# Optimization experiments

Hardware: AMD Instinct MI355X
Metric: run time of the kernel (lower is better)

The kernel has to match this reference:

```python
import jax, jax.numpy as jnp
import numpy as np


def _conv(x, w, b, pad):
    o = jax.lax.conv_general_dilated(x, w, (1, 1), [(pad, pad), (pad, pad)],
                                     dimension_numbers=('NCHW', 'OIHW', 'NCHW'))
    return o + b[None, :, None, None]


def _prelu(x, a):
    return jnp.where(x >= 0, x, a * x)


def _bn(x, g, b):
    # training-mode BatchNorm2d (biased variance, eps=1e-5)
    m = jnp.mean(x, axis=(0, 2, 3), keepdims=True)
    v = jnp.var(x, axis=(0, 2, 3), keepdims=True)
    return (x - m) * jax.lax.rsqrt(v + 1e-5) * g[None, :, None, None] + b[None, :, None, None]


def _maxpool2(x):
    return jax.lax.reduce_window(x, -jnp.inf, jax.lax.max, (1, 1, 2, 2), (1, 1, 2, 2), 'VALID')


def _up2(x):
    # bilinear upsample x2, align_corners=True
    B, C, H, W = x.shape
    Ho, Wo = 2 * H, 2 * W
    ys = jnp.arange(Ho, dtype=x.dtype) * ((H - 1) / (Ho - 1))
    xs = jnp.arange(Wo, dtype=x.dtype) * ((W - 1) / (Wo - 1))
    y0 = jnp.floor(ys).astype(jnp.int32)
    y1 = jnp.minimum(y0 + 1, H - 1)
    wy = (ys - y0.astype(x.dtype))[:, None]
    x0 = jnp.floor(xs).astype(jnp.int32)
    x1 = jnp.minimum(x0 + 1, W - 1)
    wx = xs - x0.astype(x.dtype)
    rows = x[:, :, y0, :] * (1 - wy) + x[:, :, y1, :] * wy  # [B,C,Ho,W]
    return rows[:, :, :, x0] * (1 - wx) + rows[:, :, :, x1] * wx


def _dyn_conv(x, w):
    # per-sample dynamic conv: x [B,1,H,W], w [B,Cout,k,k], pad = k//2 - 1
    # fused as a single grouped conv (groups = B) instead of B*Cout tiny launches
    B, Cout, k, _ = w.shape
    pad = k // 2 - 1
    xi = x.reshape(1, B, x.shape[2], x.shape[3])
    wi = w.reshape(B * Cout, 1, k, k)
    o = jax.lax.conv_general_dilated(xi, wi, (1, 1), [(pad, pad), (pad, pad)],
                                     dimension_numbers=('NCHW', 'OIHW', 'NCHW'),
                                     feature_group_count=B)
    return o.reshape(B, Cout, o.shape[2], o.shape[3])


def _double(x, w1, b1, w2, b2, a1, a2):
    return _prelu(_conv(_prelu(_conv(x, w1, b1, 1), a1), w2, b2, 1), a2)


def _forward(x, w, c1_w, c1_b, d2_w1, d2_b1, d2_w2, d2_b2, d3_w1, d3_b1, d3_w2, d3_b2,
             d4_w1, d4_b1, d4_w2, d4_b2, u3_w1, u3_b1, u3_w2, u3_b2, u2_w1, u2_b1,
             u2_w2, u2_b2, u1_w1, u1_b1, u1_w2, u1_b2, last_w, last_b,
             bn1_g, bn1_b, bn2_g, bn2_b, bn3_g, bn3_b, bn4_g, bn4_b, prelu_a):
    c1 = _prelu(_dyn_conv(x, w), prelu_a[0])          # [B,32,H-1,W-1]
    c1 = _prelu(_conv(c1, c1_w, c1_b, 2), prelu_a[1])  # 4x4 pad 2 -> [B,32,H,W]
    c1 = _bn(c1, bn1_g, bn1_b)
    h = _maxpool2(c1)
    c2 = _bn(_double(h, d2_w1, d2_b1, d2_w2, d2_b2, prelu_a[2], prelu_a[3]), bn2_g, bn2_b)
    h = _maxpool2(c2)
    c3 = _bn(_double(h, d3_w1, d3_b1, d3_w2, d3_b2, prelu_a[4], prelu_a[5]), bn3_g, bn3_b)
    h = _maxpool2(c3)
    h = _bn(_double(h, d4_w1, d4_b1, d4_w2, d4_b2, prelu_a[6], prelu_a[7]), bn4_g, bn4_b)
    h = jnp.concatenate([_up2(h), c3], axis=1)  # 512+256
    h = _double(h, u3_w1, u3_b1, u3_w2, u3_b2, prelu_a[8], prelu_a[9])
    h = jnp.concatenate([_up2(h), c2], axis=1)  # 256+128
    h = _double(h, u2_w1, u2_b1, u2_w2, u2_b2, prelu_a[10], prelu_a[11])
    h = jnp.concatenate([_up2(h), c1], axis=1)  # 128+32
    h = _double(h, u1_w1, u1_b1, u1_w2, u1_b2, prelu_a[12], prelu_a[13])
    return _conv(h, last_w, last_b, 0)


def setup_inputs() -> dict:
    key = jax.random.key(0)
    ks = iter(jax.random.split(key, 32))
    d = {}
    d['x'] = jax.random.normal(next(ks), (8, 1, 256, 256), jnp.float32)
    d['w'] = jax.random.normal(next(ks), (8, 32, 8, 8), jnp.float32) * 0.1
    wspecs = [('c1_w', (32, 32, 4, 4)), ('d2_w1', (128, 32, 3, 3)), ('d2_w2', (128, 128, 3, 3)),
              ('d3_w1', (256, 128, 3, 3)), ('d3_w2', (256, 256, 3, 3)),
              ('d4_w1', (512, 256, 3, 3)), ('d4_w2', (512, 512, 3, 3)),
              ('u3_w1', (256, 768, 3, 3)), ('u3_w2', (256, 256, 3, 3)),
              ('u2_w1', (128, 384, 3, 3)), ('u2_w2', (128, 128, 3, 3)),
              ('u1_w1', (32, 160, 3, 3)), ('u1_w2', (32, 32, 3, 3)), ('last_w', (1, 32, 1, 1))]
    for name, shp in wspecs:
        d[name] = jax.random.normal(next(ks), shp, jnp.float32) * 0.05
        d[name.replace('_w', '_b')] = jnp.zeros((shp[0],), jnp.float32)
    for name, c in [('bn1', 32), ('bn2', 128), ('bn3', 256), ('bn4', 512)]:
        d[name + '_g'] = jnp.ones((c,), jnp.float32)
        d[name + '_b'] = jnp.zeros((c,), jnp.float32)
    d['prelu_a'] = jnp.full((14,), 0.25, jnp.float32)
    return d


def reference(x, w, c1_w, c1_b, d2_w1, d2_b1, d2_w2, d2_b2, d3_w1, d3_b1, d3_w2, d3_b2,
              d4_w1, d4_b1, d4_w2, d4_b2, u3_w1, u3_b1, u3_w2, u3_b2, u2_w1, u2_b1,
              u2_w2, u2_b2, u1_w1, u1_b1, u1_w2, u1_b2, last_w, last_b,
              bn1_g, bn1_b, bn2_g, bn2_b, bn3_g, bn3_b, bn4_g, bn4_b, prelu_a):
    return _forward(x, w, c1_w, c1_b, d2_w1, d2_b1, d2_w2, d2_b2, d3_w1, d3_b1,
                    d3_w2, d3_b2, d4_w1, d4_b1, d4_w2, d4_b2, u3_w1, u3_b1, u3_w2,
                    u3_b2, u2_w1, u2_b1, u2_w2, u2_b2, u1_w1, u1_b1, u1_w2, u1_b2,
                    last_w, last_b, bn1_g, bn1_b, bn2_g, bn2_b, bn3_g, bn3_b,
                    bn4_g, bn4_b, prelu_a)
```

## Files before the change

### kernel.cpp

```cpp
#include <hip/hip_runtime.h>
#include <hip/hip_bf16.h>
#include <cstddef>


typedef _Float16 h16;
typedef __attribute__((ext_vector_type(8))) _Float16 h16x8;
typedef __attribute__((ext_vector_type(4))) float f32x4;
union F8 { uint4 u; h16x8 h; };
union UH { unsigned u; h16 h[2]; };

__device__ __forceinline__ float h2f(unsigned short s) {
    union { h16 h; unsigned short s; } c; c.s = s; return (float)c.h;
}
__device__ __forceinline__ unsigned short f2h(float f) {
    union { h16 h; unsigned short s; } c; c.h = (h16)f; return c.s;
}
__device__ __forceinline__ unsigned pack2(float a, float b) {
    return (unsigned)f2h(a) | ((unsigned)f2h(b) << 16);
}
__device__ __forceinline__ void up8(const uint4& v, float* f) {
    f[0]=h2f(v.x&0xffff); f[1]=h2f(v.x>>16);
    f[2]=h2f(v.y&0xffff); f[3]=h2f(v.y>>16);
    f[4]=h2f(v.z&0xffff); f[5]=h2f(v.z>>16);
    f[6]=h2f(v.w&0xffff); f[7]=h2f(v.w>>16);
}

struct PackDesc { const float* src; h16* dst; int I, T, OB, nGrp; };
struct PackArgs { PackDesc d[13]; int total; };

__global__ __launch_bounds__(256) void k_packall(PackArgs a)
{
    int gid = blockIdx.x * 256 + threadIdx.x;
    if (gid >= a.total) return;
    int li = 0, rel = gid;
    while (rel >= a.d[li].nGrp) { rel -= a.d[li].nGrp; ++li; }
    const PackDesc& D = a.d[li];
    int I8 = D.I >> 3;
    int o  = rel / (D.T * I8);
    int r2 = rel - o * (D.T * I8);
    int t  = r2 / I8;
    int i8 = r2 - t * I8;
    int ob = o / D.OB, om = o - ob * D.OB;
    int mt = om >> 4, m16 = om & 15;
    int chunk = i8 >> 2, quad = i8 & 3;
    int lane = quad * 16 + m16;
    int nch = D.I >> 5;
    size_t grp = ((((size_t)ob * D.T + t) * nch + chunk) * (D.OB >> 4) + mt) * 64 + lane;
    const float* src = D.src + ((size_t)o * D.I + i8 * 8) * D.T + t;
    h16* d = D.dst + grp * 8;
#pragma unroll
    for (int j = 0; j < 8; ++j) d[j] = (h16)src[(size_t)j * D.T];
}

template<int KH, int KW, int PAD, bool UPS, int MT, bool FIN>
__global__ __launch_bounds__(256, 2) void k_conv_mfma(
    const h16* __restrict__ src1, int C1n, int H1, int W1,
    const h16* __restrict__ src2, int C2n,
    int Hin, int Win, int Ho, int Wo,
    const h16* __restrict__ PW, const float* __restrict__ bias,
    const float* __restrict__ pa, int aidx,
    h16* __restrict__ out, int Cout,
    const float* __restrict__ fw, const float* __restrict__ fb,
    float* __restrict__ fout)
{
    constexpr int WINH = 8 + KH - 1, WINW = 32 + KW - 1;
    constexpr int NPIX = WINH * WINW;
    constexpr int NIT  = NPIX * 4;
    constexpr int MAXIT = (NIT + 255) / 256;
    constexpr int TAPS = KH * KW;
    __shared__ unsigned short lds[2][NPIX * 36];

    const int tid = threadIdx.x;
    const int lane = tid & 63, wv = tid >> 6;
    const int quad = lane >> 4, m16 = lane & 15;
    const int nCb = Cout / (16 * MT);
    const int b  = blockIdx.z / nCb, cb = blockIdx.z % nCb;
    const int x0 = blockIdx.x * 32, y0 = blockIdx.y * 8;
    const int Cin = C1n + C2n;
    const int nch = Cin >> 5;
    const int co_base = cb * (16 * MT);
    const int srcH = UPS ? Hin : H1;
    const int srcW = UPS ? Win : W1;

    int lof[MAXIT];
    int g1[MAXIT];
    int fl[MAXIT];
    unsigned fyfx[MAXIT];
    int g2[MAXIT];

    const float ry = UPS ? (float)(H1 - 1) / (float)(Hin - 1) : 0.f;
    const float rx = UPS ? (float)(W1 - 1) / (float)(Win - 1) : 0.f;
    const int W1C = UPS ? W1 * C1n : 0;

#pragma unroll
    for (int it = 0; it < MAXIT; ++it) {
        int i = tid + it * 256;
        if (i >= NIT) { lof[it] = -1; g1[it] = -1; g2[it] = -1; fl[it] = 0; fyfx[it] = 0; continue; }
        int p = i >> 2, q = i & 3;
        int wy = p / WINW, wx = p - wy * WINW;
        int yy = y0 - PAD + wy, xx = x0 - PAD + wx;
        lof[it] = p * 36 + q * 8;
        bool val = (unsigned)yy < (unsigned)srcH && (unsigned)xx < (unsigned)srcW;
        if (UPS) {
            fl[it] = 0; fyfx[it] = 0; g1[it] = -1; g2[it] = -1;
            if (val) {
                float ys = yy * ry, xs = xx * rx;
                int yl0 = (int)ys, xl0 = (int)xs;
                float fy = ys - (float)yl0, fx = xs - (float)xl0;
                g1[it] = ((b * H1 + yl0) * W1 + xl0) * C1n + q * 8;
                fl[it] = (yl0 < H1 - 1 ? 1 : 0) | (xl0 < W1 - 1 ? 2 : 0);
                fyfx[it] = pack2(fy, fx);
                g2[it] = ((b * Hin + yy) * Win + xx) * C2n + q * 8;
            }
        } else {
            fl[it] = 0; fyfx[it] = 0; g2[it] = -1;
            g1[it] = val ? ((b * H1 + yy) * W1 + xx) * C1n + q * 8 : -1;
        }
    }

    f32x4 acc[MT][4];
#pragma unroll
    for (int i = 0; i < MT; ++i)
#pragma unroll
        for (int j = 0; j < 4; ++j) acc[i][j] = (f32x4){0.f, 0.f, 0.f, 0.f};

    auto stage = [&](int c0, unsigned short* buf) {
        if (UPS && c0 < C1n) {
#pragma unroll
            for (int it = 0; it < MAXIT; ++it) {
                int lo = lof[it];
                if (lo < 0) continue;
                uint2 lo8 = {0u, 0u}, hi8 = {0u, 0u};
                int g = g1[it];
                if (g >= 0) {
                    const h16* p00 = src1 + g + c0;
                    int oy = (fl[it] & 1) ? W1C : 0;
                    int ox = (fl[it] & 2) ? C1n : 0;
                    F8 v00, v01, v10, v11;
                    v00.u = *(const uint4*)(p00);
                    v01.u = *(const uint4*)(p00 + ox);
                    v10.u = *(const uint4*)(p00 + oy);
                    v11.u = *(const uint4*)(p00 + oy + ox);
                    UH t; t.u = fyfx[it];
                    h16 fy = t.h[0], fx = t.h[1];
                    h16x8 r0 = v00.h + (v10.h - v00.h) * fy;
                    h16x8 r1 = v01.h + (v11.h - v01.h) * fy;
                    F8 rr; rr.h = r0 + (r1 - r0) * fx;
                    lo8 = make_uint2(rr.u.x, rr.u.y);
                    hi8 = make_uint2(rr.u.z, rr.u.w);
                }
                *(uint2*)&buf[lo] = lo8;
                *(uint2*)&buf[lo + 4] = hi8;
            }
        } else if (UPS) {
            int cs = c0 - C1n;
#pragma unroll
            for (int it = 0; it < MAXIT; ++it) {
                int lo = lof[it];
                if (lo < 0) continue;
                uint4 v = {0u, 0u, 0u, 0u};
                int g = g2[it];
                if (g >= 0) v = *(const uint4*)(src2 + g + cs);
                *(uint2*)&buf[lo] = make_uint2(v.x, v.y);
                *(uint2*)&buf[lo + 4] = make_uint2(v.z, v.w);
            }
        } else {
#pragma unroll
            for (int it = 0; it < MAXIT; ++it) {
                int lo = lof[it];
                if (lo < 0) continue;
                uint4 v = {0u, 0u, 0u, 0u};
                int g = g1[it];
                if (g >= 0) v = *(const uint4*)(src1 + g + c0);
                *(uint2*)&buf[lo] = make_uint2(v.x, v.y);
                *(uint2*)&buf[lo + 4] = make_uint2(v.z, v.w);
            }
        }
    };

    const uint4* PW4 = (const uint4*)PW;
    auto sweep = [&](int ci, const unsigned short* buf) {
        size_t abase = (((size_t)cb * TAPS) * nch + ci) * (MT * 64) + lane;
        const size_t astep = (size_t)nch * (MT * 64);
#pragma unroll
        for (int kx = 0; kx < KW; ++kx) {
            F8 a[KH][MT];
#pragma unroll
            for (int ky = 0; ky < KH; ++ky)
#pragma unroll
                for (int mt = 0; mt < MT; ++mt)
                    a[ky][mt].u = PW4[abase + (size_t)(ky * KW + kx) * astep + mt * 64];
#pragma unroll
            for (int wr = 0; wr < 2 + KH - 1; ++wr) {
#pragma unroll
                for (int cg = 0; cg < 2; ++cg) {
                    int row = (wv << 1) + wr;
                    int col = (cg << 4) + m16;
                    int li = (row * WINW + col + kx) * 36 + quad * 8;
                    F8 bf;
                    ((uint2*)&bf)[0] = *(const uint2*)&buf[li];
                    ((uint2*)&bf)[1] = *(const uint2*)&buf[li + 4];
#pragma unroll
                    for (int ky = 0; ky < KH; ++ky) {
                        int ntr = wr - ky;
                        if (ntr < 0 || ntr > 1) continue;
                        int nt = (ntr << 1) + cg;
#pragma unroll
                        for (int mt = 0; mt < MT; ++mt)
                            acc[mt][nt] = __builtin_amdgcn_mfma_f32_16x16x32_f16(
                                a[ky][mt].h, bf.h, acc[mt][nt], 0, 0, 0);
                    }
                }
            }
        }
    };

    stage(0, lds[0]);
    __syncthreads();
    for (int ci = 0; ci < nch; ++ci) {
        int p = ci & 1;
        if (ci + 1 < nch) stage((ci + 1) << 5, lds[p ^ 1]);
        sweep(ci, lds[p]);
        __syncthreads();
    }

    const float alpha = pa[aidx];
    float fin_acc[4] = {0.f, 0.f, 0.f, 0.f};
#pragma unroll
    for (int mt = 0; mt < MT; ++mt) {
        int co = co_base + mt * 16 + quad * 4;
        float4 bi = *(const float4*)(bias + co);
        float4 fw4 = {0.f, 0.f, 0.f, 0.f};
        if (FIN) fw4 = *(const float4*)(fw + co);
#pragma unroll
        for (int nt = 0; nt < 4; ++nt) {
            int y = y0 + (wv << 1) + (nt >> 1);
            int x = x0 + ((nt & 1) << 4) + m16;
            float v0 = acc[mt][nt][0] + bi.x;
            float v1 = acc[mt][nt][1] + bi.y;
            float v2 = acc[mt][nt][2] + bi.z;
            float v3 = acc[mt][nt][3] + bi.w;
            v0 = v0 >= 0.f ? v0 : alpha * v0;
            v1 = v1 >= 0.f ? v1 : alpha * v1;
            v2 = v2 >= 0.f ? v2 : alpha * v2;
            v3 = v3 >= 0.f ? v3 : alpha * v3;
            if (FIN) {
                fin_acc[nt] += v0 * fw4.x + v1 * fw4.y + v2 * fw4.z + v3 * fw4.w;
            } else {
                uint2 r; r.x = pack2(v0, v1); r.y = pack2(v2, v3);
                *(uint2*)(out + ((size_t)((b * Ho + y) * Wo + x)) * Cout + co) = r;
            }
        }
    }
    if (FIN) {
        float fb0 = fb[0];
#pragma unroll
        for (int nt = 0; nt < 4; ++nt) {
            float p = fin_acc[nt];
            p += __shfl_xor(p, 16);
            p += __shfl_xor(p, 32);
            if (quad == 0) {
                int y = y0 + (wv << 1) + (nt >> 1);
                int x = x0 + ((nt & 1) << 4) + m16;
                fout[(size_t)(b * Ho + y) * Wo + x] = p + fb0;
            }
        }
    }
}

__global__ __launch_bounds__(256) void k_dynconv(
    const float* __restrict__ x,
    const float* __restrict__ w,
    const float* __restrict__ pa,
    h16* __restrict__ out)
{
    __shared__ float wl[2048];
    int b = blockIdx.y;
    for (int j = threadIdx.x; j < 2048; j += 256) {
        int t = j >> 5, co = j & 31;
        wl[j] = w[((size_t)(b * 32 + co)) * 64 + t];
    }
    __syncthreads();
    int idx = blockIdx.x * 256 + threadIdx.x;
    if (idx >= 65025) return;
    int py = idx / 255, px = idx - py * 255;
    float acc[32];
#pragma unroll
    for (int c = 0; c < 32; ++c) acc[c] = 0.f;
    const float* xp = x + (size_t)b * 65536;
#pragma unroll
    for (int ky = 0; ky < 8; ++ky) {
        int iy = py + ky - 3;
        if ((unsigned)iy >= 256u) continue;
        const float* row = xp + iy * 256;
#pragma unroll
        for (int kx = 0; kx < 8; ++kx) {
            int ix = px + kx - 3;
            if ((unsigned)ix >= 256u) continue;
            float v = row[ix];
            const float4* wr = (const float4*)&wl[(ky * 8 + kx) * 32];
#pragma unroll
            for (int cg = 0; cg < 8; ++cg) {
                float4 wv = wr[cg];
                acc[cg*4+0] += v * wv.x; acc[cg*4+1] += v * wv.y;
                acc[cg*4+2] += v * wv.z; acc[cg*4+3] += v * wv.w;
            }
        }
    }
    float a = pa[0];
    h16* op = out + ((size_t)(b * 65025 + idx)) * 32;
#pragma unroll
    for (int cg = 0; cg < 4; ++cg) {
        float v[8];
#pragma unroll
        for (int k = 0; k < 8; ++k) {
            float t = acc[cg * 8 + k];
            v[k] = t >= 0.f ? t : a * t;
        }
        uint4 r;
        r.x = pack2(v[0], v[1]); r.y = pack2(v[2], v[3]);
        r.z = pack2(v[4], v[5]); r.w = pack2(v[6], v[7]);
        *(uint4*)(op + cg * 8) = r;
    }
}

__global__ __launch_bounds__(256) void k_bnstats(
    const h16* __restrict__ x, int C, int N, float* __restrict__ sums)
{
    __shared__ float ls[1024];
    for (int j = threadIdx.x; j < 2 * C; j += 256) ls[j] = 0.f;
    __syncthreads();
    int start = blockIdx.x * 256 + threadIdx.x;
    int stride = gridDim.x * 256;
    int c = start & (C - 1);
    float s = 0.f, q = 0.f;
    for (int i = start; i < N; i += stride) {
        float v = h2f(((const unsigned short*)x)[i]);
        s += v; q += v * v;
    }
    atomicAdd(&ls[c], s);
    atomicAdd(&ls[C + c], q);
    __syncthreads();
    for (int j = threadIdx.x; j < 2 * C; j += 256) atomicAdd(&sums[j], ls[j]);
}

__global__ void k_bnfin(
    const float* __restrict__ sums, const float* __restrict__ g,
    const float* __restrict__ bta, int C, float invN, float* __restrict__ sc)
{
    int c = threadIdx.x;
    if (c >= C) return;
    float mean = sums[c] * invN;
    float var  = sums[C + c] * invN - mean * mean;
    float s    = g[c] / sqrtf(var + 1e-5f);
    sc[c]      = s;
    sc[C + c]  = bta[c] - mean * s;
}

__global__ __launch_bounds__(256) void k_bnapply_pool(
    h16* __restrict__ x, h16* __restrict__ pooled,
    int Hin, int Win, int C, int lc8, int lwo, int count,
    const float* __restrict__ sc)
{
    int idx = blockIdx.x * 256 + threadIdx.x;
    if (idx >= count) return;
    int b = blockIdx.y;
    int c8 = idx & ((1 << lc8) - 1);
    int t  = idx >> lc8;
    int ox = t & ((1 << lwo) - 1);
    int oy = t >> lwo;
    int cb = c8 * 8;
    float s[8], sh[8];
#pragma unroll
    for (int k = 0; k < 8; ++k) { s[k] = sc[cb + k]; sh[k] = sc[C + cb + k]; }
    h16* p = x + ((size_t)((b * Hin + oy * 2) * Win + ox * 2)) * C + cb;
    size_t rs = (size_t)Win * C;
    uint4 v00 = *(const uint4*)p;
    uint4 v01 = *(const uint4*)(p + C);
    uint4 v10 = *(const uint4*)(p + rs);
    uint4 v11 = *(const uint4*)(p + rs + C);
    float a[8], bb[8], c[8], d[8], m[8];
    up8(v00, a); up8(v01, bb); up8(v10, c); up8(v11, d);
#pragma unroll
    for (int k = 0; k < 8; ++k) {
        a[k]  = a[k]  * s[k] + sh[k];
        bb[k] = bb[k] * s[k] + sh[k];
        c[k]  = c[k]  * s[k] + sh[k];
        d[k]  = d[k]  * s[k] + sh[k];
        m[k]  = fmaxf(fmaxf(a[k], bb[k]), fmaxf(c[k], d[k]));
    }
    uint4 r;
    r.x = pack2(a[0],a[1]);  r.y = pack2(a[2],a[3]);  r.z = pack2(a[4],a[5]);  r.w = pack2(a[6],a[7]);
    *(uint4*)p = r;
    r.x = pack2(bb[0],bb[1]); r.y = pack2(bb[2],bb[3]); r.z = pack2(bb[4],bb[5]); r.w = pack2(bb[6],bb[7]);
    *(uint4*)(p + C) = r;
    r.x = pack2(c[0],c[1]);  r.y = pack2(c[2],c[3]);  r.z = pack2(c[4],c[5]);  r.w = pack2(c[6],c[7]);
    *(uint4*)(p + rs) = r;
    r.x = pack2(d[0],d[1]);  r.y = pack2(d[2],d[3]);  r.z = pack2(d[4],d[5]);  r.w = pack2(d[6],d[7]);
    *(uint4*)(p + rs + C) = r;
    r.x = pack2(m[0],m[1]);  r.y = pack2(m[2],m[3]);  r.z = pack2(m[4],m[5]);  r.w = pack2(m[6],m[7]);
    int Wo = 1 << lwo;
    *(uint4*)(pooled + ((size_t)((b * (Hin >> 1) + oy)) * Wo + ox) * C + cb) = r;
}

__global__ __launch_bounds__(256) void k_bnapply(
    h16* __restrict__ x, int C, int N8, const float* __restrict__ sc)
{
    __shared__ float ls[1024];
    for (int j = threadIdx.x; j < 2 * C; j += 256) ls[j] = sc[j];
    __syncthreads();
    int idx = blockIdx.x * 256 + threadIdx.x;
    if (idx >= N8) return;
    int cb = (idx << 3) & (C - 1);
    h16* p = x + (size_t)idx * 8;
    uint4 v = *(const uint4*)p;
    float f[8];
    up8(v, f);
    uint4 r;
    float o[8];
#pragma unroll
    for (int k = 0; k < 8; ++k) o[k] = f[k] * ls[cb + k] + ls[C + cb + k];
    r.x = pack2(o[0], o[1]); r.y = pack2(o[2], o[3]);
    r.z = pack2(o[4], o[5]); r.w = pack2(o[6], o[7]);
    *(uint4*)p = r;
}

extern "C" void kernel_launch(void* const* d_in, const int* in_sizes, int n_in,
                              void* d_out, int out_size, void* d_ws, size_t ws_size,
                              hipStream_t stream)
{
    const float* x      = (const float*)d_in[0];
    const float* w      = (const float*)d_in[1];
    const float* c1_w   = (const float*)d_in[2];
    const float* c1_b   = (const float*)d_in[3];
    const float* d2_w1  = (const float*)d_in[4];
    const float* d2_b1  = (const float*)d_in[5];
    const float* d2_w2  = (const float*)d_in[6];
    const float* d2_b2  = (const float*)d_in[7];
    const float* d3_w1  = (const float*)d_in[8];
    const float* d3_b1  = (const float*)d_in[9];
    const float* d3_w2  = (const float*)d_in[10];
    const float* d3_b2  = (const float*)d_in[11];
    const float* d4_w1  = (const float*)d_in[12];
    const float* d4_b1  = (const float*)d_in[13];
    const float* d4_w2  = (const float*)d_in[14];
    const float* d4_b2  = (const float*)d_in[15];
    const float* u3_w1  = (const float*)d_in[16];
    const float* u3_b1  = (const float*)d_in[17];
    const float* u3_w2  = (const float*)d_in[18];
    const float* u3_b2  = (const float*)d_in[19];
    const float* u2_w1  = (const float*)d_in[20];
    const float* u2_b1  = (const float*)d_in[21];
    const float* u2_w2  = (const float*)d_in[22];
    const float* u2_b2  = (const float*)d_in[23];
    const float* u1_w1  = (const float*)d_in[24];
    const float* u1_b1  = (const float*)d_in[25];
    const float* u1_w2  = (const float*)d_in[26];
    const float* u1_b2  = (const float*)d_in[27];
    const float* last_w = (const float*)d_in[28];
    const float* last_b = (const float*)d_in[29];
    const float* bn1_g  = (const float*)d_in[30];
    const float* bn1_b  = (const float*)d_in[31];
    const float* bn2_g  = (const float*)d_in[32];
    const float* bn2_b  = (const float*)d_in[33];
    const float* bn3_g  = (const float*)d_in[34];
    const float* bn3_b  = (const float*)d_in[35];
    const float* bn4_g  = (const float*)d_in[36];
    const float* bn4_b  = (const float*)d_in[37];
    const float* pa     = (const float*)d_in[38];
    float* out = (float*)d_out;

    h16* A0 = (h16*)d_ws;
    h16* C1 = A0;
    h16* C2 = A0 + 16777216;
    h16* C3 = A0 + 33554432;
    h16* A  = A0 + 41943040;
    h16* B  = A0 + 58720256;
    h16* PWb= A0 + 75497472;
    float* SUMS = (float*)(A0 + 83126272);
    float* SC   = SUMS + 2048;
    size_t need = (size_t)83126272 * 2 + 3072 * 4;
    if (ws_size < need) return;

    h16* pw_c1   = PWb;
    h16* pw_d2w1 = PWb + 16384;
    h16* pw_d2w2 = PWb + 53248;
    h16* pw_d3w1 = PWb + 200704;
    h16* pw_d3w2 = PWb + 495616;
    h16* pw_d4w1 = PWb + 1085440;
    h16* pw_d4w2 = PWb + 2265088;
    h16* pw_u3w1 = PWb + 4624384;
    h16* pw_u3w2 = PWb + 6393856;
    h16* pw_u2w1 = PWb + 6983680;
    h16* pw_u2w2 = PWb + 7426048;
    h16* pw_u1w1 = PWb + 7573504;
    h16* pw_u1w2 = PWb + 7619584;

    dim3 blk(256);

    hipMemsetAsync(SUMS, 0, 2048 * sizeof(float), stream);

    PackArgs pk;
    auto mk = [](const float* s, h16* d, int I, int T, int O, int OB) {
        return PackDesc{s, d, I, T, OB, (I >> 3) * T * O};
    };
    pk.d[0]  = mk(c1_w,  pw_c1,   32, 16, 32, 32);
    pk.d[1]  = mk(d2_w1, pw_d2w1, 32,  9, 128, 64);
    pk.d[2]  = mk(d2_w2, pw_d2w2, 128, 9, 128, 64);
    pk.d[3]  = mk(d3_w1, pw_d3w1, 128, 9, 256, 64);
    pk.d[4]  = mk(d3_w2, pw_d3w2, 256, 9, 256, 64);
    pk.d[5]  = mk(d4_w1, pw_d4w1, 256, 9, 512, 32);
    pk.d[6]  = mk(d4_w2, pw_d4w2, 512, 9, 512, 32);
    pk.d[7]  = mk(u3_w1, pw_u3w1, 768, 9, 256, 64);
    pk.d[8]  = mk(u3_w2, pw_u3w2, 256, 9, 256, 64);
    pk.d[9]  = mk(u2_w1, pw_u2w1, 384, 9, 128, 64);
    pk.d[10] = mk(u2_w2, pw_u2w2, 128, 9, 128, 64);
    pk.d[11] = mk(u1_w1, pw_u1w1, 160, 9, 32, 32);
    pk.d[12] = mk(u1_w2, pw_u1w2, 32,  9, 32, 32);
    pk.total = 0;
    for (int i = 0; i < 13; ++i) pk.total += pk.d[i].nGrp;
    k_packall<<<dim3((pk.total + 255) / 256), blk, 0, stream>>>(pk);

    const float* NF = nullptr;
    float* NFO = nullptr;

    k_dynconv<<<dim3(255, 8), blk, 0, stream>>>(x, w, pa, A);
    k_conv_mfma<4,4,2,false,2,false><<<dim3(8, 32, 8), blk, 0, stream>>>(
        A, 32, 255, 255, nullptr, 0, 255, 255, 256, 256,
        pw_c1, c1_b, pa, 1, C1, 32, NF, NF, NFO);
    k_bnstats<<<dim3(1024), blk, 0, stream>>>(C1, 32, 16777216, SUMS);
    k_bnfin<<<dim3(1), dim3(512), 0, stream>>>(SUMS, bn1_g, bn1_b, 32, 32.f / 16777216.f, SC);
    k_bnapply_pool<<<dim3(256, 8), blk, 0, stream>>>(C1, B, 256, 256, 32, 2, 7, 65536, SC);

    k_conv_mfma<3,3,1,false,4,false><<<dim3(4, 16, 16), blk, 0, stream>>>(
        B, 32, 128, 128, nullptr, 0, 128, 128, 128, 128,
        pw_d2w1, d2_b1, pa, 2, A, 128, NF, NF, NFO);
    k_conv_mfma<3,3,1,false,4,false><<<dim3(4, 16, 16), blk, 0, stream>>>(
        A, 128, 128, 128, nullptr, 0, 128, 128, 128, 128,
        pw_d2w2, d2_b2, pa, 3, C2, 128, NF, NF, NFO);
    k_bnstats<<<dim3(1024), blk, 0, stream>>>(C2, 128, 16777216, SUMS + 64);
    k_bnfin<<<dim3(1), dim3(512), 0, stream>>>(SUMS + 64, bn2_g, bn2_b, 128, 128.f / 16777216.f, SC);
    k_bnapply_pool<<<dim3(256, 8), blk, 0, stream>>>(C2, B, 128, 128, 128, 4, 6, 65536, SC);

    k_conv_mfma<3,3,1,false,4,false><<<dim3(2, 8, 32), blk, 0, stream>>>(
        B, 128, 64, 64, nullptr, 0, 64, 64, 64, 64,
        pw_d3w1, d3_b1, pa, 4, A, 256, NF, NF, NFO);
    k_conv_mfma<3,3,1,false,4,false><<<dim3(2, 8, 32), blk, 0, stream>>>(
        A, 256, 64, 64, nullptr, 0, 64, 64, 64, 64,
        pw_d3w2, d3_b2, pa, 5, C3, 256, NF, NF, NFO);
    k_bnstats<<<dim3(1024), blk, 0, stream>>>(C3, 256, 8388608, SUMS + 320);
    k_bnfin<<<dim3(1), dim3(512), 0, stream>>>(SUMS + 320, bn3_g, bn3_b, 256, 256.f / 8388608.f, SC);
    k_bnapply_pool<<<dim3(128, 8), blk, 0, stream>>>(C3, B, 64, 64, 256, 5, 5, 32768, SC);

    k_conv_mfma<3,3,1,false,2,false><<<dim3(1, 4, 128), blk, 0, stream>>>(
        B, 256, 32, 32, nullptr, 0, 32, 32, 32, 32,
        pw_d4w1, d4_b1, pa, 6, A, 512, NF, NF, NFO);
    k_conv_mfma<3,3,1,false,2,false><<<dim3(1, 4, 128), blk, 0, stream>>>(
        A, 512, 32, 32, nullptr, 0, 32, 32, 32, 32,
        pw_d4w2, d4_b2, pa, 7, B, 512, NF, NF, NFO);
    k_bnstats<<<dim3(1024), blk, 0, stream>>>(B, 512, 4194304, SUMS + 832);
    k_bnfin<<<dim3(1), dim3(512), 0, stream>>>(SUMS + 832, bn4_g, bn4_b, 512, 512.f / 4194304.f, SC);
    k_bnapply<<<dim3(2048), blk, 0, stream>>>(B, 512, 524288, SC);

    k_conv_mfma<3,3,1,true,4,false><<<dim3(2, 8, 32), blk, 0, stream>>>(
        B, 512, 32, 32, C3, 256, 64, 64, 64, 64,
        pw_u3w1, u3_b1, pa, 8, A, 256, NF, NF, NFO);
    k_conv_mfma<3,3,1,false,4,false><<<dim3(2, 8, 32), blk, 0, stream>>>(
        A, 256, 64, 64, nullptr, 0, 64, 64, 64, 64,
        pw_u3w2, u3_b2, pa, 9, B, 256, NF, NF, NFO);

    k_conv_mfma<3,3,1,true,4,false><<<dim3(4, 16, 16), blk, 0, stream>>>(
        B, 256, 64, 64, C2, 128, 128, 128, 128, 128,
        pw_u2w1, u2_b1, pa, 10, A, 128, NF, NF, NFO);
    k_conv_mfma<3,3,1,false,4,false><<<dim3(4, 16, 16), blk, 0, stream>>>(
        A, 128, 128, 128, nullptr, 0, 128, 128, 128, 128,
        pw_u2w2, u2_b2, pa, 11, B, 128, NF, NF, NFO);

    k_conv_mfma<3,3,1,true,2,false><<<dim3(8, 32, 8), blk, 0, stream>>>(
        B, 128, 128, 128, C1, 32, 256, 256, 256, 256,
        pw_u1w1, u1_b1, pa, 12, A, 32, NF, NF, NFO);
    k_conv_mfma<3,3,1,false,2,true><<<dim3(8, 32, 8), blk, 0, stream>>>(
        A, 32, 256, 256, nullptr, 0, 256, 256, 256, 256,
        pw_u1w2, u1_b2, pa, 13, B, 32, last_w, last_b, out);
}
```

Before: 1.186 ms.

## Fuse BatchNorm statistics into conv epilogue and fold finalize into apply kernels

The conv kernel gains a BNS template flag. When it is set, the epilogue accumulates per-channel sum and sum of squares of the post-PReLU outputs, reduces them with wave shuffles and LDS atomics, then adds them to global sums with atomics. This removes four separate bnstats passes that reread large fp16 activations, and the bnfin launches are folded into the apply kernels, which now compute scale and shift per thread. In exchange the epilogue carries extra registers and atomics, and every apply thread redundantly recomputes sqrt and divide. Statistics are now summed in fp32 before fp16 rounding, which changes numerics slightly.

```diff
diff --git a/kernel.cpp b/kernel.cpp
--- a/kernel.cpp
+++ b/kernel.cpp
@@ -52,7 +52,7 @@
     for (int j = 0; j < 8; ++j) d[j] = (h16)src[(size_t)j * D.T];
 }
 
-template<int KH, int KW, int PAD, bool UPS, int MT, bool FIN>
+template<int KH, int KW, int PAD, bool UPS, int MT, bool FIN, bool BNS>
 __global__ __launch_bounds__(256, 2) void k_conv_mfma(
     const h16* __restrict__ src1, int C1n, int H1, int W1,
     const h16* __restrict__ src2, int C2n,
@@ -61,7 +61,7 @@
     const float* __restrict__ pa, int aidx,
     h16* __restrict__ out, int Cout,
     const float* __restrict__ fw, const float* __restrict__ fb,
-    float* __restrict__ fout)
+    float* __restrict__ fout, float* __restrict__ gsums)
 {
     constexpr int WINH = 8 + KH - 1, WINW = 32 + KW - 1;
     constexpr int NPIX = WINH * WINW;
@@ -69,6 +69,7 @@
     constexpr int MAXIT = (NIT + 255) / 256;
     constexpr int TAPS = KH * KW;
     __shared__ unsigned short lds[2][NPIX * 36];
+    __shared__ float bnred[128];
 
     const int tid = threadIdx.x;
     const int lane = tid & 63, wv = tid >> 6;
@@ -216,6 +217,7 @@
     };
 
     stage(0, lds[0]);
+    if (BNS && tid < 128) bnred[tid] = 0.f;
     __syncthreads();
     for (int ci = 0; ci < nch; ++ci) {
         int p = ci & 1;
@@ -226,6 +228,13 @@
 
     const float alpha = pa[aidx];
     float fin_acc[4] = {0.f, 0.f, 0.f, 0.f};
+    float lsum[MT][4], lsq[MT][4];
+    if (BNS) {
+#pragma unroll
+        for (int mt = 0; mt < MT; ++mt)
+#pragma unroll
+            for (int j = 0; j < 4; ++j) { lsum[mt][j] = 0.f; lsq[mt][j] = 0.f; }
+    }
 #pragma unroll
     for (int mt = 0; mt < MT; ++mt) {
         int co = co_base + mt * 16 + quad * 4;
@@ -244,6 +253,12 @@
             v1 = v1 >= 0.f ? v1 : alpha * v1;
             v2 = v2 >= 0.f ? v2 : alpha * v2;
             v3 = v3 >= 0.f ? v3 : alpha * v3;
+            if (BNS) {
+                lsum[mt][0] += v0; lsq[mt][0] += v0 * v0;
+                lsum[mt][1] += v1; lsq[mt][1] += v1 * v1;
+                lsum[mt][2] += v2; lsq[mt][2] += v2 * v2;
+                lsum[mt][3] += v3; lsq[mt][3] += v3 * v3;
+            }
             if (FIN) {
                 fin_acc[nt] += v0 * fw4.x + v1 * fw4.y + v2 * fw4.z + v3 * fw4.w;
             } else {
@@ -264,6 +279,30 @@
                 int x = x0 + ((nt & 1) << 4) + m16;
                 fout[(size_t)(b * Ho + y) * Wo + x] = p + fb0;
             }
+        }
+    }
+    if (BNS) {
+#pragma unroll
+        for (int mt = 0; mt < MT; ++mt)
+#pragma unroll
+            for (int j = 0; j < 4; ++j) {
+                float s = lsum[mt][j], q = lsq[mt][j];
+                s += __shfl_xor(s, 1); q += __shfl_xor(q, 1);
+                s += __shfl_xor(s, 2); q += __shfl_xor(q, 2);
+                s += __shfl_xor(s, 4); q += __shfl_xor(q, 4);
+                s += __shfl_xor(s, 8); q += __shfl_xor(q, 8);
+                if (m16 == 0) {
+                    int ch = mt * 16 + quad * 4 + j;
+                    atomicAdd(&bnred[ch], s);
+                    atomicAdd(&bnred[64 + ch], q);
+                }
+            }
+        __syncthreads();
+        if (tid < 16 * MT)
+            atomicAdd(&gsums[co_base + tid], bnred[tid]);
+        else if (tid < 32 * MT) {
+            int ch = tid - 16 * MT;
+            atomicAdd(&gsums[Cout + co_base + ch], bnred[64 + ch]);
         }
     }
 }
@@ -324,43 +363,11 @@
     }
 }
 
-__global__ __launch_bounds__(256) void k_bnstats(
-    const h16* __restrict__ x, int C, int N, float* __restrict__ sums)
-{
-    __shared__ float ls[1024];
-    for (int j = threadIdx.x; j < 2 * C; j += 256) ls[j] = 0.f;
-    __syncthreads();
-    int start = blockIdx.x * 256 + threadIdx.x;
-    int stride = gridDim.x * 256;
-    int c = start & (C - 1);
-    float s = 0.f, q = 0.f;
-    for (int i = start; i < N; i += stride) {
-        float v = h2f(((const unsigned short*)x)[i]);
-        s += v; q += v * v;
-    }
-    atomicAdd(&ls[c], s);
-    atomicAdd(&ls[C + c], q);
-    __syncthreads();
-    for (int j = threadIdx.x; j < 2 * C; j += 256) atomicAdd(&sums[j], ls[j]);
-}
-
-__global__ void k_bnfin(
-    const float* __restrict__ sums, const float* __restrict__ g,
-    const float* __restrict__ bta, int C, float invN, float* __restrict__ sc)
-{
-    int c = threadIdx.x;
-    if (c >= C) return;
-    float mean = sums[c] * invN;
-    float var  = sums[C + c] * invN - mean * mean;
-    float s    = g[c] / sqrtf(var + 1e-5f);
-    sc[c]      = s;
-    sc[C + c]  = bta[c] - mean * s;
-}
-
 __global__ __launch_bounds__(256) void k_bnapply_pool(
     h16* __restrict__ x, h16* __restrict__ pooled,
     int Hin, int Win, int C, int lc8, int lwo, int count,
-    const float* __restrict__ sc)
+    const float* __restrict__ sums, const float* __restrict__ g,
+    const float* __restrict__ beta, float invN)
 {
     int idx = blockIdx.x * 256 + threadIdx.x;
     if (idx >= count) return;
@@ -372,7 +379,14 @@
     int cb = c8 * 8;
     float s[8], sh[8];
 #pragma unroll
-    for (int k = 0; k < 8; ++k) { s[k] = sc[cb + k]; sh[k] = sc[C + cb + k]; }
+    for (int k = 0; k < 8; ++k) {
+        int c = cb + k;
+        float mean = sums[c] * invN;
+        float var  = sums[C + c] * invN - mean * mean;
+        float sc   = g[c] / sqrtf(var + 1e-5f);
+        s[k]  = sc;
+        sh[k] = beta[c] - mean * sc;
+    }
     h16* p = x + ((size_t)((b * Hin + oy * 2) * Win + ox * 2)) * C + cb;
     size_t rs = (size_t)Win * C;
     uint4 v00 = *(const uint4*)p;
@@ -404,14 +418,23 @@
 }
 
 __global__ __launch_bounds__(256) void k_bnapply(
-    h16* __restrict__ x, int C, int N8, const float* __restrict__ sc)
+    h16* __restrict__ x, int C, int N8,
+    const float* __restrict__ sums, const float* __restrict__ g,
+    const float* __restrict__ beta, float invN)
 {
-    __shared__ float ls[1024];
-    for (int j = threadIdx.x; j < 2 * C; j += 256) ls[j] = sc[j];
-    __syncthreads();
     int idx = blockIdx.x * 256 + threadIdx.x;
     if (idx >= N8) return;
     int cb = (idx << 3) & (C - 1);
+    float s[8], sh[8];
+#pragma unroll
+    for (int k = 0; k < 8; ++k) {
+        int c = cb + k;
+        float mean = sums[c] * invN;
+        float var  = sums[C + c] * invN - mean * mean;
+        float sc   = g[c] / sqrtf(var + 1e-5f);
+        s[k]  = sc;
+        sh[k] = beta[c] - mean * sc;
+    }
     h16* p = x + (size_t)idx * 8;
     uint4 v = *(const uint4*)p;
     float f[8];
@@ -419,7 +442,7 @@
     uint4 r;
     float o[8];
 #pragma unroll
-    for (int k = 0; k < 8; ++k) o[k] = f[k] * ls[cb + k] + ls[C + cb + k];
+    for (int k = 0; k < 8; ++k) o[k] = f[k] * s[k] + sh[k];
     r.x = pack2(o[0], o[1]); r.y = pack2(o[2], o[3]);
     r.z = pack2(o[4], o[5]); r.w = pack2(o[6], o[7]);
     *(uint4*)p = r;
@@ -478,8 +501,7 @@
     h16* B  = A0 + 58720256;
     h16* PWb= A0 + 75497472;
     float* SUMS = (float*)(A0 + 83126272);
-    float* SC   = SUMS + 2048;
-    size_t need = (size_t)83126272 * 2 + 3072 * 4;
+    size_t need = (size_t)83126272 * 2 + 2048 * 4;
     if (ws_size < need) return;
 
     h16* pw_c1   = PWb;
@@ -496,8 +518,9 @@
     h16* pw_u1w1 = PWb + 7573504;
     h16* pw_u1w2 = PWb + 7619584;
 
+    float* S1 = SUMS, *S2 = SUMS + 64, *S3 = SUMS + 320, *S4 = SUMS + 832;
+
     dim3 blk(256);
-
     hipMemsetAsync(SUMS, 0, 2048 * sizeof(float), stream);
 
     PackArgs pk;
@@ -525,61 +548,57 @@
     float* NFO = nullptr;
 
     k_dynconv<<<dim3(255, 8), blk, 0, stream>>>(x, w, pa, A);
-    k_conv_mfma<4,4,2,false,2,false><<<dim3(8, 32, 8), blk, 0, stream>>>(
+    k_conv_mfma<4,4,2,false,2,false,true><<<dim3(8, 32, 8), blk, 0, stream>>>(
         A, 32, 255, 255, nullptr, 0, 255, 255, 256, 256,
-        pw_c1, c1_b, pa, 1, C1, 32, NF, NF, NFO);
-    k_bnstats<<<dim3(1024), blk, 0, stream>>>(C1, 32, 16777216, SUMS);
-    k_bnfin<<<dim3(1), dim3(512), 0, stream>>>(SUMS, bn1_g, bn1_b, 32, 32.f / 16777216.f, SC);
-    k_bnapply_pool<<<dim3(256, 8), blk, 0, stream>>>(C1, B, 256, 256, 32, 2, 7, 65536, SC);
-
-    k_conv_mfma<3,3,1,false,4,false><<<dim3(4, 16, 16), blk, 0, stream>>>(
+        pw_c1, c1_b, pa, 1, C1, 32, NF, NF, NFO, S1);
+    k_bnapply_pool<<<dim3(256, 8), blk, 0, stream>>>(
+        C1, B, 256, 256, 32, 2, 7, 65536, S1, bn1_g, bn1_b, 32.f / 16777216.f);
+
+    k_conv_mfma<3,3,1,false,4,false,false><<<dim3(4, 16, 16), blk, 0, stream>>>(
         B, 32, 128, 128, nullptr, 0, 128, 128, 128, 128,
-        pw_d2w1, d2_b1, pa, 2, A, 128, NF, NF, NFO);
-    k_conv_mfma<3,3,1,false,4,false><<<dim3(4, 16, 16), blk, 0, stream>>>(
+        pw_d2w1, d2_b1, pa, 2, A, 128, NF, NF, NFO, NFO);
+    k_conv_mfma<3,3,1,false,4,false,true><<<dim3(4, 16, 16), blk, 0, stream>>>(
         A, 128, 128, 128, nullptr, 0, 128, 128, 128, 128,
-        pw_d2w2, d2_b2, pa, 3, C2, 128, NF, NF, NFO);
-    k_bnstats<<<dim3(1024), blk, 0, stream>>>(C2, 128, 16777216, SUMS + 64);
-    k_bnfin<<<dim3(1), dim3(512), 0, stream>>>(SUMS + 64, bn2_g, bn2_b, 128, 128.f / 16777216.f, SC);
-    k_bnapply_pool<<<dim3(256, 8), blk, 0, stream>>>(C2, B, 128, 128, 128, 4, 6, 65536, SC);
-
-    k_conv_mfma<3,3,1,false,4,false><<<dim3(2, 8, 32), blk, 0, stream>>>(
+        pw_d2w2, d2_b2, pa, 3, C2, 128, NF, NF, NFO, S2);
+    k_bnapply_pool<<<dim3(256, 8), blk, 0, stream>>>(
+        C2, B, 128, 128, 128, 4, 6, 65536, S2, bn2_g, bn2_b, 128.f / 16777216.f);
+
+    k_conv_mfma<3,3,1,false,4,false,false><<<dim3(2, 8, 32), blk, 0, stream>>>(
         B, 128, 64, 64, nullptr, 0, 64, 64, 64, 64,
-        pw_d3w1, d3_b1, pa, 4, A, 256, NF, NF, NFO);
-    k_conv_mfma<3,3,1,false,4,false><<<dim3(2, 8, 32), blk, 0, stream>>>(
+        pw_d3w1, d3_b1, pa, 4, A, 256, NF, NF, NFO, NFO);
+    k_conv_mfma<3,3,1,false,4,false,true><<<dim3(2, 8, 32), blk, 0, stream>>>(
         A, 256, 64, 64, nullptr, 0, 64, 64, 64, 64,
-        pw_d3w2, d3_b2, pa, 5, C3, 256, NF, NF, NFO);
-    k_bnstats<<<dim3(1024), blk, 0, stream>>>(C3, 256, 8388608, SUMS + 320);
-    k_bnfin<<<dim3(1), dim3(512), 0, stream>>>(SUMS + 320, bn3_g, bn3_b, 256, 256.f / 8388608.f, SC);
-    k_bnapply_pool<<<dim3(128, 8), blk, 0, stream>>>(C3, B, 64, 64, 256, 5, 5, 32768, SC);
-
-    k_conv_mfma<3,3,1,false,2,false><<<dim3(1, 4, 128), blk, 0, stream>>>(
+        pw_d3w2, d3_b2, pa, 5, C3, 256, NF, NF, NFO, S3);
+    k_bnapply_pool<<<dim3(128, 8), blk, 0, stream>>>(
+        C3, B, 64, 64, 256, 5, 5, 32768, S3, bn3_g, bn3_b, 256.f / 8388608.f);
+
+    k_conv_mfma<3,3,1,false,2,false,false><<<dim3(1, 4, 128), blk, 0, stream>>>(
         B, 256, 32, 32, nullptr, 0, 32, 32, 32, 32,
-        pw_d4w1, d4_b1, pa, 6, A, 512, NF, NF, NFO);
-    k_conv_mfma<3,3,1,false,2,false><<<dim3(1, 4, 128), blk, 0, stream>>>(
+        pw_d4w1, d4_b1, pa, 6, A, 512, NF, NF, NFO, NFO);
+    k_conv_mfma<3,3,1,false,2,false,true><<<dim3(1, 4, 128), blk, 0, stream>>>(
         A, 512, 32, 32, nullptr, 0, 32, 32, 32, 32,
-        pw_d4w2, d4_b2, pa, 7, B, 512, NF, NF, NFO);
-    k_bnstats<<<dim3(1024), blk, 0, stream>>>(B, 512, 4194304, SUMS + 832);
-    k_bnfin<<<dim3(1), dim3(512), 0, stream>>>(SUMS + 832, bn4_g, bn4_b, 512, 512.f / 4194304.f, SC);
-    k_bnapply<<<dim3(2048), blk, 0, stream>>>(B, 512, 524288, SC);
-
-    k_conv_mfma<3,3,1,true,4,false><<<dim3(2, 8, 32), blk, 0, stream>>>(
+        pw_d4w2, d4_b2, pa, 7, B, 512, NF, NF, NFO, S4);
+    k_bnapply<<<dim3(2048), blk, 0, stream>>>(
+        B, 512, 524288, S4, bn4_g, bn4_b, 512.f / 4194304.f);
+
+    k_conv_mfma<3,3,1,true,4,false,false><<<dim3(2, 8, 32), blk, 0, stream>>>(
         B, 512, 32, 32, C3, 256, 64, 64, 64, 64,
-        pw_u3w1, u3_b1, pa, 8, A, 256, NF, NF, NFO);
-    k_conv_mfma<3,3,1,false,4,false><<<dim3(2, 8, 32), blk, 0, stream>>>(
+        pw_u3w1, u3_b1, pa, 8, A, 256, NF, NF, NFO, NFO);
+    k_conv_mfma<3,3,1,false,4,false,false><<<dim3(2, 8, 32), blk, 0, stream>>>(
         A, 256, 64, 64, nullptr, 0, 64, 64, 64, 64,
-        pw_u3w2, u3_b2, pa, 9, B, 256, NF, NF, NFO);
-
-    k_conv_mfma<3,3,1,true,4,false><<<dim3(4, 16, 16), blk, 0, stream>>>(
+        pw_u3w2, u3_b2, pa, 9, B, 256, NF, NF, NFO, NFO);
+
+    k_conv_mfma<3,3,1,true,4,false,false><<<dim3(4, 16, 16), blk, 0, stream>>>(
         B, 256, 64, 64, C2, 128, 128, 128, 128, 128,
-        pw_u2w1, u2_b1, pa, 10, A, 128, NF, NF, NFO);
-    k_conv_mfma<3,3,1,false,4,false><<<dim3(4, 16, 16), blk, 0, stream>>>(
+        pw_u2w1, u2_b1, pa, 10, A, 128, NF, NF, NFO, NFO);
+    k_conv_mfma<3,3,1,false,4,false,false><<<dim3(4, 16, 16), blk, 0, stream>>>(
         A, 128, 128, 128, nullptr, 0, 128, 128, 128, 128,
-        pw_u2w2, u2_b2, pa, 11, B, 128, NF, NF, NFO);
-
-    k_conv_mfma<3,3,1,true,2,false><<<dim3(8, 32, 8), blk, 0, stream>>>(
+        pw_u2w2, u2_b2, pa, 11, B, 128, NF, NF, NFO, NFO);
+
+    k_conv_mfma<3,3,1,true,2,false,false><<<dim3(8, 32, 8), blk, 0, stream>>>(
         B, 128, 128, 128, C1, 32, 256, 256, 256, 256,
-        pw_u1w1, u1_b1, pa, 12, A, 32, NF, NF, NFO);
-    k_conv_mfma<3,3,1,false,2,true><<<dim3(8, 32, 8), blk, 0, stream>>>(
+        pw_u1w1, u1_b1, pa, 12, A, 32, NF, NF, NFO, NFO);
+    k_conv_mfma<3,3,1,false,2,true,false><<<dim3(8, 32, 8), blk, 0, stream>>>(
         A, 32, 256, 256, nullptr, 0, 256, 256, 256, 256,
-        pw_u1w2, u1_b2, pa, 13, B, 32, last_w, last_b, out);
-}
+        pw_u1w2, u1_b2, pa, 13, B, 32, last_w, last_b, out, NFO);
+}
```

Result: faster. 1.087 ms (-8.3%).
